# Kernel optimization log

Measured on AMD Instinct MI355X. Metric: run time of the kernel, lower is better.

## Reference

```python
import jax, jax.numpy as jnp
import numpy as np

N_NODES = 50000   # rows of x / output of NF-spmm
M_NODES = 50000   # output of FN-spmm
N_EDGES = 800000
NFEAT, N_HIDDEN, NCLASS = 300, 256, 20
N_IDX = 5000


def setup_inputs() -> dict:
    key = jax.random.key(0)
    ks = jax.random.split(key, 12)
    x = jax.random.normal(ks[0], (N_NODES, NFEAT), dtype=jnp.float32)
    fn_rows = jax.random.randint(ks[1], (N_EDGES,), 0, M_NODES)
    fn_cols = jax.random.randint(ks[2], (N_EDGES,), 0, N_NODES)
    fn_vals = jax.random.uniform(ks[3], (N_EDGES,), dtype=jnp.float32)
    nf_rows = jax.random.randint(ks[4], (N_EDGES,), 0, N_NODES)
    nf_cols = jax.random.randint(ks[5], (N_EDGES,), 0, M_NODES)
    nf_vals = jax.random.uniform(ks[6], (N_EDGES,), dtype=jnp.float32)
    idx = jax.random.randint(ks[7], (N_IDX,), 0, N_NODES)
    # learned parameters (pygcn-style GraphConvolution: spmm(adj, x @ W) + b)
    W1 = jax.random.normal(ks[8], (NFEAT, N_HIDDEN), dtype=jnp.float32) / np.sqrt(NFEAT)
    b1 = jnp.zeros((N_HIDDEN,), dtype=jnp.float32)
    W2 = jax.random.normal(ks[9], (N_HIDDEN, NCLASS), dtype=jnp.float32) / np.sqrt(N_HIDDEN)
    b2 = jnp.zeros((NCLASS,), dtype=jnp.float32)
    return {"x": x, "fn_rows": fn_rows, "fn_cols": fn_cols, "fn_vals": fn_vals,
            "nf_rows": nf_rows, "nf_cols": nf_cols, "nf_vals": nf_vals,
            "idx": idx, "W1": W1, "b1": b1, "W2": W2, "b2": b2}


def _spmm(rows, cols, vals, dense, n_out):
    # sparse(COO) @ dense: gather source rows, scale by edge value, scatter-add.
    return jax.ops.segment_sum(vals[:, None] * dense[cols], rows, num_segments=n_out)


def reference(x, fn_rows, fn_cols, fn_vals, nf_rows, nf_cols, nf_vals, idx, W1, b1, W2, b2):
    # gc1: FN @ (x @ W1) + b1, then relu  (dropout is identity in eval mode)
    h = jax.nn.relu(_spmm(fn_rows, fn_cols, fn_vals, x @ W1, M_NODES) + b1)
    # gc2: NF @ (h @ W2) + b2
    logits = _spmm(nf_rows, nf_cols, nf_vals, h @ W2, N_NODES) + b2
    return jax.nn.softmax(logits, axis=1)[idx]
```

## Files before the change

### kernel.cpp

```cpp
#include <hip/hip_runtime.h>

#define N_NODES 50000
#define M_NODES 50000
#define N_EDGES 800000
#define NFEAT   300
#define NHID    256
#define NCLASS  20
#define N_IDX   5000
#define KTILES  10
#define NTOT    (M_NODES + N_NODES)

typedef __attribute__((ext_vector_type(8))) short bf16x8;
typedef __attribute__((ext_vector_type(4))) float f32x4;

__device__ inline unsigned short f2bf(float f) {
    unsigned u = __float_as_uint(f);
    u += 0x7fff + ((u >> 16) & 1);
    return (unsigned short)(u >> 16);
}
__device__ inline float bf2f(unsigned short h) { return __uint_as_float((unsigned)h << 16); }
__device__ inline float bflo(unsigned v) { return __uint_as_float(v << 16); }
__device__ inline float bfhi(unsigned v) { return __uint_as_float(v & 0xffff0000u); }

__global__ __launch_bounds__(256) void prep_w1_mark_kernel(const float* __restrict__ W1,
                                                           unsigned short* __restrict__ w1h,
                                                           unsigned short* __restrict__ w1l,
                                                           const int* __restrict__ idx,
                                                           int* __restrict__ mark) {
    if (blockIdx.x < 320) {
        int id = blockIdx.x * 256 + threadIdx.x;
        int col = id & 255;
        int k   = id >> 8;
        float v = (k < NFEAT) ? W1[(size_t)k * NHID + col] : 0.f;
        unsigned short hi = f2bf(v);
        unsigned short lo = f2bf(v - bf2f(hi));
        size_t off = (size_t)(k >> 5) * (256 * 32) + (size_t)col * 32 + (k & 31);
        w1h[off] = hi;
        w1l[off] = lo;
    } else {
        int i = (blockIdx.x - 320) * 256 + threadIdx.x;
        if (i < N_IDX) mark[idx[i]] = 1;
    }
}

__global__ __launch_bounds__(256) void gemm1_mfma_kernel(const float* __restrict__ x,
                                                         const unsigned short* __restrict__ w1h,
                                                         const unsigned short* __restrict__ w1l,
                                                         unsigned short* __restrict__ xwb) {
    __shared__ unsigned short Ah[2][64 * 40];
    __shared__ unsigned short Al[2][64 * 40];

    const int tid  = threadIdx.x;
    const int lane = tid & 63;
    const int wv   = tid >> 6;
    const int l15  = lane & 15;
    const int g    = lane >> 4;
    const int row0 = blockIdx.x * 64;

    const int sr = tid >> 2;
    const int sc = tid & 3;
    const bool rowok = (row0 + sr) < N_NODES;
    const float* __restrict__ xrow = x + (size_t)(row0 + sr) * NFEAT;

    float cur[8], nxt[8];
    if (rowok) {
        float4 v0 = *(const float4*)&xrow[sc * 8 + 0];
        float4 v1 = *(const float4*)&xrow[sc * 8 + 4];
        cur[0] = v0.x; cur[1] = v0.y; cur[2] = v0.z; cur[3] = v0.w;
        cur[4] = v1.x; cur[5] = v1.y; cur[6] = v1.z; cur[7] = v1.w;
    } else {
#pragma unroll
        for (int j = 0; j < 8; ++j) cur[j] = 0.f;
    }

    f32x4 acc[4][4];
#pragma unroll
    for (int mf = 0; mf < 4; ++mf)
#pragma unroll
        for (int nf = 0; nf < 4; ++nf) acc[mf][nf] = (f32x4){0.f, 0.f, 0.f, 0.f};

    for (int t = 0; t < KTILES; ++t) {
        if (t < KTILES - 1) {
            const int k0 = (t + 1) * 32 + sc * 8;
            if (t + 1 < KTILES - 1) {
                if (rowok) {
                    float4 v0 = *(const float4*)&xrow[k0 + 0];
                    float4 v1 = *(const float4*)&xrow[k0 + 4];
                    nxt[0] = v0.x; nxt[1] = v0.y; nxt[2] = v0.z; nxt[3] = v0.w;
                    nxt[4] = v1.x; nxt[5] = v1.y; nxt[6] = v1.z; nxt[7] = v1.w;
                } else {
#pragma unroll
                    for (int j = 0; j < 8; ++j) nxt[j] = 0.f;
                }
            } else {
#pragma unroll
                for (int j = 0; j < 8; ++j) {
                    int k = k0 + j;
                    nxt[j] = (rowok && k < NFEAT) ? xrow[k] : 0.f;
                }
            }
        }

        {
            bf16x8 hv, lv;
#pragma unroll
            for (int j = 0; j < 8; ++j) {
                unsigned short h = f2bf(cur[j]);
                hv[j] = (short)h;
                lv[j] = (short)f2bf(cur[j] - bf2f(h));
            }
            const int wo = sr * 40 + sc * 8;
            *(bf16x8*)&Ah[t & 1][wo] = hv;
            *(bf16x8*)&Al[t & 1][wo] = lv;
        }
        __syncthreads();

        const int b = t & 1;
        bf16x8 ah[4], al[4];
#pragma unroll
        for (int mf = 0; mf < 4; ++mf) {
            const int ao = (mf * 16 + l15) * 40 + g * 8;
            ah[mf] = *(const bf16x8*)&Ah[b][ao];
            al[mf] = *(const bf16x8*)&Al[b][ao];
        }
        bf16x8 bh[4], bl[4];
#pragma unroll
        for (int nf = 0; nf < 4; ++nf) {
            const size_t bo = (size_t)t * 8192 + (size_t)(wv * 64 + nf * 16 + l15) * 32 + g * 8;
            bh[nf] = *(const bf16x8*)&w1h[bo];
            bl[nf] = *(const bf16x8*)&w1l[bo];
        }
#pragma unroll
        for (int mf = 0; mf < 4; ++mf)
#pragma unroll
            for (int nf = 0; nf < 4; ++nf) {
                acc[mf][nf] = __builtin_amdgcn_mfma_f32_16x16x32_bf16(ah[mf], bh[nf], acc[mf][nf], 0, 0, 0);
                acc[mf][nf] = __builtin_amdgcn_mfma_f32_16x16x32_bf16(ah[mf], bl[nf], acc[mf][nf], 0, 0, 0);
                acc[mf][nf] = __builtin_amdgcn_mfma_f32_16x16x32_bf16(al[mf], bh[nf], acc[mf][nf], 0, 0, 0);
            }
#pragma unroll
        for (int j = 0; j < 8; ++j) cur[j] = nxt[j];
    }

    const int colb = wv * 64;
#pragma unroll
    for (int mf = 0; mf < 4; ++mf) {
        const int rg0 = row0 + mf * 16 + g * 4;
#pragma unroll
        for (int nf = 0; nf < 4; ++nf) {
            const int cg = colb + nf * 16 + l15;
#pragma unroll
            for (int j = 0; j < 4; ++j) {
                const int rg = rg0 + j;
                if (rg < N_NODES) xwb[(size_t)rg * NHID + cg] = f2bf(acc[mf][nf][j]);
            }
        }
    }
}

__global__ __launch_bounds__(256) void hist_both_kernel(const int* __restrict__ fn_rows,
                                                        const int* __restrict__ nf_rows,
                                                        const int* __restrict__ mark,
                                                        int* __restrict__ counts,
                                                        unsigned short* __restrict__ fn_rank,
                                                        unsigned short* __restrict__ nf_rank) {
    const int base = blockIdx.x * 1024 + threadIdx.x;
    int r[4], r2[4], m2[4];
#pragma unroll
    for (int k = 0; k < 4; ++k) {
        int e = base + k * 256;
        r[k]  = (e < N_EDGES) ? fn_rows[e] : -1;
        r2[k] = (e < N_EDGES) ? nf_rows[e] : -1;
    }
#pragma unroll
    for (int k = 0; k < 4; ++k) m2[k] = (r2[k] >= 0) ? mark[r2[k]] : 0;
#pragma unroll
    for (int k = 0; k < 4; ++k) {
        if (r[k] >= 0) {
            int p = atomicAdd(&counts[r[k]], 1);
            fn_rank[base + k * 256] = (unsigned short)p;
        }
    }
#pragma unroll
    for (int k = 0; k < 4; ++k) {
        if (m2[k]) {
            int p = atomicAdd(&counts[M_NODES + r2[k]], 1);
            nf_rank[base + k * 256] = (unsigned short)p;
        }
    }
}

__global__ __launch_bounds__(256) void scan_chunk_kernel(const int* __restrict__ counts,
                                                         int* __restrict__ chunk_incl,
                                                         int* __restrict__ chunk_sums, int n) {
    __shared__ int lds[256];
    int i = blockIdx.x * 256 + threadIdx.x;
    int v = (i < n) ? counts[i] : 0;
    lds[threadIdx.x] = v;
    __syncthreads();
    for (int off = 1; off < 256; off <<= 1) {
        int t = (threadIdx.x >= off) ? lds[threadIdx.x - off] : 0;
        __syncthreads();
        lds[threadIdx.x] += t;
        __syncthreads();
    }
    if (i < n) chunk_incl[i] = lds[threadIdx.x];
    if (threadIdx.x == 255) chunk_sums[blockIdx.x] = lds[255];
}

__global__ __launch_bounds__(512) void scan_sums_kernel(const int* __restrict__ chunk_sums,
                                                        int* __restrict__ chunk_off,
                                                        int* __restrict__ row_ptr_end, int nchunks) {
    __shared__ int lds[512];
    int tid = threadIdx.x;
    int v = (tid < nchunks) ? chunk_sums[tid] : 0;
    lds[tid] = v;
    __syncthreads();
    for (int off = 1; off < 512; off <<= 1) {
        int t = (tid >= off) ? lds[tid - off] : 0;
        __syncthreads();
        lds[tid] += t;
        __syncthreads();
    }
    if (tid < nchunks) chunk_off[tid] = lds[tid] - v;
    if (tid == nchunks - 1) *row_ptr_end = lds[tid];
}

__global__ void scan_apply_kernel(const int* __restrict__ counts,
                                  const int* __restrict__ chunk_incl,
                                  const int* __restrict__ chunk_off,
                                  int* __restrict__ row_ptr, int n) {
    int i = blockIdx.x * 256 + threadIdx.x;
    if (i < n) row_ptr[i] = chunk_incl[i] - counts[i] + chunk_off[blockIdx.x];
}

__global__ __launch_bounds__(256) void scatter_both_kernel(const int* __restrict__ fn_rows,
                                                           const int* __restrict__ fn_cols,
                                                           const float* __restrict__ fn_vals,
                                                           const int* __restrict__ nf_rows,
                                                           const int* __restrict__ nf_cols,
                                                           const float* __restrict__ nf_vals,
                                                           const int* __restrict__ mark,
                                                           const int* __restrict__ row_ptr,
                                                           const unsigned short* __restrict__ fn_rank,
                                                           const unsigned short* __restrict__ nf_rank,
                                                           uint2* __restrict__ csr_cv) {
    const int base = blockIdx.x * 1024 + threadIdx.x;
#pragma unroll
    for (int k = 0; k < 4; ++k) {
        int e = base + k * 256;
        if (e < N_EDGES) {
            int r = fn_rows[e];
            int p = row_ptr[r] + fn_rank[e];
            csr_cv[p] = make_uint2((unsigned)fn_cols[e], __float_as_uint(fn_vals[e]));
        }
    }
#pragma unroll
    for (int k = 0; k < 4; ++k) {
        int e = base + k * 256;
        if (e < N_EDGES) {
            int r2 = nf_rows[e];
            if (mark[r2]) {
                int p = row_ptr[M_NODES + r2] + nf_rank[e];
                csr_cv[p] = make_uint2((unsigned)nf_cols[e], __float_as_uint(nf_vals[e]));
            }
        }
    }
}

__global__ __launch_bounds__(128) void spmm_fn_kernel(const int* __restrict__ row_ptr,
                                                      const uint2* __restrict__ csr_cv,
                                                      const unsigned* __restrict__ xwb,
                                                      const float* __restrict__ b1,
                                                      unsigned* __restrict__ hb) {
    const int r = blockIdx.x;
    const int t = threadIdx.x;
    const int s = row_ptr[r], e = row_ptr[r + 1];
    float a0 = 0.f, a1 = 0.f;
    for (int j0 = s; j0 < e; j0 += 8) {
        uint2 cv[8];
        unsigned xv[8];
#pragma unroll
        for (int k = 0; k < 8; ++k)
            cv[k] = (j0 + k < e) ? csr_cv[j0 + k] : make_uint2(0u, 0u);
#pragma unroll
        for (int k = 0; k < 8; ++k)
            xv[k] = (j0 + k < e) ? xwb[(size_t)cv[k].x * 128 + t] : 0u;
#pragma unroll
        for (int k = 0; k < 8; ++k) {
            float v = __uint_as_float(cv[k].y);
            a0 += v * bflo(xv[k]);
            a1 += v * bfhi(xv[k]);
        }
    }
    float2 bv = *(const float2*)&b1[t * 2];
    float o0 = fmaxf(a0 + bv.x, 0.f);
    float o1 = fmaxf(a1 + bv.y, 0.f);
    hb[(size_t)r * 128 + t] = ((unsigned)f2bf(o1) << 16) | (unsigned)f2bf(o0);
}

__global__ __launch_bounds__(256) void gemm2_kernel(const uint4* __restrict__ hb,
                                                    const float* __restrict__ W2,
                                                    float* __restrict__ hw) {
    __shared__ float w2s[NHID * NCLASS];
    for (int i = threadIdx.x; i < NHID * NCLASS; i += 256) w2s[i] = W2[i];
    __syncthreads();
    int gid = blockIdx.x * 256 + threadIdx.x;
    if (gid >= N_NODES * NCLASS) return;
    int row = gid / NCLASS;
    int col = gid - row * NCLASS;
    const uint4* hp = &hb[(size_t)row * 32];
    float acc = 0.f;
#pragma unroll 4
    for (int k8 = 0; k8 < 32; ++k8) {
        uint4 hv = hp[k8];
        int k = k8 * 8;
        acc += bflo(hv.x) * w2s[(k + 0) * NCLASS + col];
        acc += bfhi(hv.x) * w2s[(k + 1) * NCLASS + col];
        acc += bflo(hv.y) * w2s[(k + 2) * NCLASS + col];
        acc += bfhi(hv.y) * w2s[(k + 3) * NCLASS + col];
        acc += bflo(hv.z) * w2s[(k + 4) * NCLASS + col];
        acc += bfhi(hv.z) * w2s[(k + 5) * NCLASS + col];
        acc += bflo(hv.w) * w2s[(k + 6) * NCLASS + col];
        acc += bfhi(hv.w) * w2s[(k + 7) * NCLASS + col];
    }
    hw[gid] = acc;
}

__global__ __launch_bounds__(64) void spmm_nf_softmax_kernel(const int* __restrict__ idx,
                                                             const int* __restrict__ row_ptr,
                                                             const uint2* __restrict__ csr_cv,
                                                             const float* __restrict__ hw,
                                                             const float* __restrict__ b2,
                                                             float* __restrict__ out) {
    const int b    = blockIdx.x;
    const int lane = threadIdx.x;
    const int r = idx[b];
    const int s = row_ptr[M_NODES + r], e = row_ptr[M_NODES + r + 1];

    float acc[NCLASS];
#pragma unroll
    for (int k = 0; k < NCLASS; ++k) acc[k] = 0.f;

    for (int j = s + lane; j < e; j += 64) {
        uint2 cv = csr_cv[j];
        int   c = (int)cv.x;
        float v = __uint_as_float(cv.y);
        const float4* hp = (const float4*)&hw[(size_t)c * NCLASS];
        float4 h0 = hp[0], h1 = hp[1], h2 = hp[2], h3 = hp[3], h4 = hp[4];
        acc[0]  += v * h0.x; acc[1]  += v * h0.y; acc[2]  += v * h0.z; acc[3]  += v * h0.w;
        acc[4]  += v * h1.x; acc[5]  += v * h1.y; acc[6]  += v * h1.z; acc[7]  += v * h1.w;
        acc[8]  += v * h2.x; acc[9]  += v * h2.y; acc[10] += v * h2.z; acc[11] += v * h2.w;
        acc[12] += v * h3.x; acc[13] += v * h3.y; acc[14] += v * h3.z; acc[15] += v * h3.w;
        acc[16] += v * h4.x; acc[17] += v * h4.y; acc[18] += v * h4.z; acc[19] += v * h4.w;
    }

#pragma unroll
    for (int k = 0; k < NCLASS; ++k) {
#pragma unroll
        for (int off = 1; off < 64; off <<= 1) acc[k] += __shfl_xor(acc[k], off, 64);
    }

    if (lane == 0) {
        float v[NCLASS];
        float m = -1e30f;
#pragma unroll
        for (int k = 0; k < NCLASS; ++k) {
            v[k] = acc[k] + b2[k];
            m = fmaxf(m, v[k]);
        }
        float sum = 0.f;
#pragma unroll
        for (int k = 0; k < NCLASS; ++k) {
            v[k] = __expf(v[k] - m);
            sum += v[k];
        }
        float inv = 1.f / sum;
#pragma unroll
        for (int k = 0; k < NCLASS; ++k) out[(size_t)b * NCLASS + k] = v[k] * inv;
    }
}

extern "C" void kernel_launch(void* const* d_in, const int* in_sizes, int n_in,
                              void* d_out, int out_size, void* d_ws, size_t ws_size,
                              hipStream_t stream) {
    const float* x       = (const float*)d_in[0];
    const int*   fn_rows = (const int*)  d_in[1];
    const int*   fn_cols = (const int*)  d_in[2];
    const float* fn_vals = (const float*)d_in[3];
    const int*   nf_rows = (const int*)  d_in[4];
    const int*   nf_cols = (const int*)  d_in[5];
    const float* nf_vals = (const float*)d_in[6];
    const int*   idx     = (const int*)  d_in[7];
    const float* W1      = (const float*)d_in[8];
    const float* b1      = (const float*)d_in[9];
    const float* W2      = (const float*)d_in[10];
    const float* b2      = (const float*)d_in[11];
    float* out = (float*)d_out;

    size_t off = 0;
    auto alloc = [&](size_t bytes) {
        void* p = (char*)d_ws + off;
        off += (bytes + 255) & ~(size_t)255;
        return p;
    };
    unsigned short* xwb = (unsigned short*)alloc((size_t)N_NODES * NHID * 2);
    unsigned*       hb  = (unsigned*)      alloc((size_t)M_NODES * NHID * 2);
    float* hw       = (float*)alloc((size_t)M_NODES * NCLASS * 4);
    int*   counts   = (int*)  alloc((size_t)NTOT * 4);
    int*   mark     = (int*)  alloc((size_t)N_NODES * 4);
    int*   row_ptr  = (int*)  alloc((size_t)(NTOT + 1) * 4);
    uint2* csr_cv   = (uint2*)alloc((size_t)2 * N_EDGES * 8);
    unsigned short* fn_rank = (unsigned short*)alloc((size_t)N_EDGES * 2);
    unsigned short* nf_rank = (unsigned short*)alloc((size_t)N_EDGES * 2);
    int*   chunk_incl = (int*)alloc((size_t)NTOT * 4);
    int*   chunk_sums = (int*)alloc(512 * 4);
    int*   chunk_off  = (int*)alloc(512 * 4);
    unsigned short* w1h = (unsigned short*)alloc((size_t)KTILES * 256 * 32 * 2);
    unsigned short* w1l = (unsigned short*)alloc((size_t)KTILES * 256 * 32 * 2);
    (void)ws_size; (void)n_in; (void)in_sizes; (void)out_size;

    const int NCHUNKS_ALL = (NTOT + 255) / 256;
    const int EB4 = (N_EDGES + 1023) / 1024;

    size_t zlen = (size_t)((char*)mark - (char*)counts) + (size_t)N_NODES * 4;
    hipMemsetAsync(counts, 0, zlen, stream);

    prep_w1_mark_kernel<<<320 + (N_IDX + 255) / 256, 256, 0, stream>>>(W1, w1h, w1l, idx, mark);

    gemm1_mfma_kernel<<<(N_NODES + 63) / 64, 256, 0, stream>>>(x, w1h, w1l, xwb);

    hist_both_kernel<<<EB4, 256, 0, stream>>>(fn_rows, nf_rows, mark, counts, fn_rank, nf_rank);
    scan_chunk_kernel<<<NCHUNKS_ALL, 256, 0, stream>>>(counts, chunk_incl, chunk_sums, NTOT);
    scan_sums_kernel<<<1, 512, 0, stream>>>(chunk_sums, chunk_off, &row_ptr[NTOT], NCHUNKS_ALL);
    scan_apply_kernel<<<NCHUNKS_ALL, 256, 0, stream>>>(counts, chunk_incl, chunk_off, row_ptr, NTOT);
    scatter_both_kernel<<<EB4, 256, 0, stream>>>(fn_rows, fn_cols, fn_vals,
                                                 nf_rows, nf_cols, nf_vals,
                                                 mark, row_ptr, fn_rank, nf_rank, csr_cv);

    spmm_fn_kernel<<<M_NODES, 128, 0, stream>>>(row_ptr, csr_cv, (const unsigned*)xwb, b1, hb);

    gemm2_kernel<<<(N_NODES * NCLASS + 255) / 256, 256, 0, stream>>>((const uint4*)hb, W2, hw);

    spmm_nf_softmax_kernel<<<N_IDX, 64, 0, stream>>>(idx, row_ptr, csr_cv, hw, b2, out);
}
```

Measured before the change: 218.3 us.

## Slice XW into 32-column panels and map each panel to one XCD in FN spmm

```diff
diff --git a/kernel.cpp b/kernel.cpp
--- a/kernel.cpp
+++ b/kernel.cpp
@@ -46,7 +46,7 @@
 __global__ __launch_bounds__(256) void gemm1_mfma_kernel(const float* __restrict__ x,
                                                          const unsigned short* __restrict__ w1h,
                                                          const unsigned short* __restrict__ w1l,
-                                                         unsigned short* __restrict__ xwb) {
+                                                         unsigned short* __restrict__ xws) {
     __shared__ unsigned short Ah[2][64 * 40];
     __shared__ unsigned short Al[2][64 * 40];
 
@@ -149,10 +149,11 @@
 #pragma unroll
         for (int nf = 0; nf < 4; ++nf) {
             const int cg = colb + nf * 16 + l15;
+            const size_t sbase = (size_t)(cg >> 5) * ((size_t)N_NODES * 32) + (cg & 31);
 #pragma unroll
             for (int j = 0; j < 4; ++j) {
-                const int rg = rg0 + j;
-                if (rg < N_NODES) xwb[(size_t)rg * NHID + cg] = f2bf(acc[mf][nf][j]);
+                const int rgj = rg0 + j;
+                if (rgj < N_NODES) xws[sbase + (size_t)rgj * 32] = f2bf(acc[mf][nf][j]);
             }
         }
     }
@@ -268,35 +269,43 @@
     }
 }
 
-__global__ __launch_bounds__(128) void spmm_fn_kernel(const int* __restrict__ row_ptr,
-                                                      const uint2* __restrict__ csr_cv,
-                                                      const unsigned* __restrict__ xwb,
-                                                      const float* __restrict__ b1,
-                                                      unsigned* __restrict__ hb) {
-    const int r = blockIdx.x;
-    const int t = threadIdx.x;
+__global__ __launch_bounds__(128) void spmm_fn_xcd_kernel(const int* __restrict__ row_ptr,
+                                                          const uint2* __restrict__ csr_cv,
+                                                          const unsigned* __restrict__ xws,
+                                                          const float* __restrict__ b1,
+                                                          unsigned* __restrict__ hb) {
+    const int bid = blockIdx.x;
+    const int rg  = bid >> 3;
+    const int p   = bid & 7;
+    const int t   = threadIdx.x;
+    const int rr  = t >> 4;
+    const int nl  = t & 15;
+    const int r   = rg * 8 + rr;
     const int s = row_ptr[r], e = row_ptr[r + 1];
+    const unsigned* __restrict__ xs = xws + (size_t)p * (N_NODES * 16) + nl;
+
     float a0 = 0.f, a1 = 0.f;
-    for (int j0 = s; j0 < e; j0 += 8) {
-        uint2 cv[8];
-        unsigned xv[8];
-#pragma unroll
-        for (int k = 0; k < 8; ++k)
+    for (int j0 = s; j0 < e; j0 += 4) {
+        uint2 cv[4];
+        unsigned xv[4];
+#pragma unroll
+        for (int k = 0; k < 4; ++k)
             cv[k] = (j0 + k < e) ? csr_cv[j0 + k] : make_uint2(0u, 0u);
 #pragma unroll
-        for (int k = 0; k < 8; ++k)
-            xv[k] = (j0 + k < e) ? xwb[(size_t)cv[k].x * 128 + t] : 0u;
-#pragma unroll
-        for (int k = 0; k < 8; ++k) {
+        for (int k = 0; k < 4; ++k)
+            xv[k] = (j0 + k < e) ? xs[(size_t)cv[k].x * 16] : 0u;
+#pragma unroll
+        for (int k = 0; k < 4; ++k) {
             float v = __uint_as_float(cv[k].y);
             a0 += v * bflo(xv[k]);
             a1 += v * bfhi(xv[k]);
         }
     }
-    float2 bv = *(const float2*)&b1[t * 2];
+    const int col2 = p * 16 + nl;
+    float2 bv = *(const float2*)&b1[col2 * 2];
     float o0 = fmaxf(a0 + bv.x, 0.f);
     float o1 = fmaxf(a1 + bv.y, 0.f);
-    hb[(size_t)r * 128 + t] = ((unsigned)f2bf(o1) << 16) | (unsigned)f2bf(o0);
+    hb[(size_t)r * 128 + col2] = ((unsigned)f2bf(o1) << 16) | (unsigned)f2bf(o0);
 }
 
 __global__ __launch_bounds__(256) void gemm2_kernel(const uint4* __restrict__ hb,
@@ -404,7 +413,7 @@
         off += (bytes + 255) & ~(size_t)255;
         return p;
     };
-    unsigned short* xwb = (unsigned short*)alloc((size_t)N_NODES * NHID * 2);
+    unsigned short* xws = (unsigned short*)alloc((size_t)N_NODES * NHID * 2);
     unsigned*       hb  = (unsigned*)      alloc((size_t)M_NODES * NHID * 2);
     float* hw       = (float*)alloc((size_t)M_NODES * NCLASS * 4);
     int*   counts   = (int*)  alloc((size_t)NTOT * 4);
@@ -428,7 +437,7 @@
 
     prep_w1_mark_kernel<<<320 + (N_IDX + 255) / 256, 256, 0, stream>>>(W1, w1h, w1l, idx, mark);
 
-    gemm1_mfma_kernel<<<(N_NODES + 63) / 64, 256, 0, stream>>>(x, w1h, w1l, xwb);
+    gemm1_mfma_kernel<<<(N_NODES + 63) / 64, 256, 0, stream>>>(x, w1h, w1l, xws);
 
     hist_both_kernel<<<EB4, 256, 0, stream>>>(fn_rows, nf_rows, mark, counts, fn_rank, nf_rank);
     scan_chunk_kernel<<<NCHUNKS_ALL, 256, 0, stream>>>(counts, chunk_incl, chunk_sums, NTOT);
@@ -438,7 +447,8 @@
                                                  nf_rows, nf_cols, nf_vals,
                                                  mark, row_ptr, fn_rank, nf_rank, csr_cv);
 
-    spmm_fn_kernel<<<M_NODES, 128, 0, stream>>>(row_ptr, csr_cv, (const unsigned*)xwb, b1, hb);
+    spmm_fn_xcd_kernel<<<(N_NODES / 8) * 8, 128, 0, stream>>>(row_ptr, csr_cv,
+                                                              (const unsigned*)xws, b1, hb);
 
     gemm2_kernel<<<(N_NODES * NCLASS + 255) / 256, 256, 0, stream>>>((const uint4*)hb, W2, hw);
 
```

After: 268.2 us. 1.23x slower.
